# Kernel optimization log

Measured on AMD Instinct MI355X. Metric: run time of the kernel, lower is better.

The kernel has to match this reference:

```python
import jax, jax.numpy as jnp
import numpy as np

B, S, D = 4, 2048, 1024
H = 16
HD = D // H

def setup_inputs() -> dict:
    key = jax.random.key(0)
    ks = jax.random.split(key, 5)
    x = jax.random.normal(ks[0], (B, S, D), dtype=jnp.float32)
    # PyTorch Linear: y = x @ W.T + b; store W in torch layout [out, in]
    w_qkv = jax.random.normal(ks[1], (3 * D, D), dtype=jnp.float32) * (1.0 / np.sqrt(D))
    b_qkv = jax.random.normal(ks[2], (3 * D,), dtype=jnp.float32) * 0.01
    w_out = jax.random.normal(ks[3], (D, D), dtype=jnp.float32) * (1.0 / np.sqrt(D))
    b_out = jax.random.normal(ks[4], (D,), dtype=jnp.float32) * 0.01
    return {"x": x, "w_qkv": w_qkv, "b_qkv": b_qkv, "w_out": w_out, "b_out": b_out}

def reference(x, w_qkv, b_qkv, w_out, b_out):
    b, s, d = x.shape
    qkv = x @ w_qkv.T + b_qkv                      # [B,S,3D]
    q, k, v = jnp.split(qkv, 3, axis=2)
    # [B,S,D] -> [B,H,S,HD]
    q = q.reshape(b, s, H, HD).transpose(0, 2, 1, 3)
    k = k.reshape(b, s, H, HD).transpose(0, 2, 1, 3)
    v = v.reshape(b, s, H, HD).transpose(0, 2, 1, 3)
    att = jnp.einsum('bhqd,bhkd->bhqk', q, k) / np.sqrt(HD)
    causal = jnp.tril(jnp.ones((s, s), dtype=bool))
    att = jnp.where(causal[None, None], att, -jnp.inf)
    att = jax.nn.softmax(att, axis=-1)
    y = jnp.einsum('bhqk,bhkd->bhqd', att, v)      # [B,H,S,HD]
    y = y.transpose(0, 2, 1, 3).reshape(b, s, d)
    return y @ w_out.T + b_out
```

## Files before the change

### kernel.cpp

```cpp
#include <hip/hip_runtime.h>
#include <hip/hip_bf16.h>

#define DEV __device__ __forceinline__

typedef __attribute__((ext_vector_type(8))) short bf16x8;
typedef __attribute__((ext_vector_type(4))) float f32x4;

#define BB 4
#define SS 2048
#define DD 1024
#define HH 16
#define HDD 64
#define MM (BB * SS)
#define NT (SS / 64)
#define NQT (SS / 128)

DEV short f2bf(float f) {
  unsigned u = __builtin_bit_cast(unsigned, f);
  u = u + 0x7fffu + ((u >> 16) & 1u);
  return (short)(u >> 16);
}

DEV float fexp2(float x) {
  float r;
  asm("v_exp_f32 %0, %1" : "=v"(r) : "v"(x));
  return r;
}
DEV float frcp(float x) {
  float r;
  asm("v_rcp_f32 %0, %1" : "=v"(r) : "v"(x));
  return r;
}
DEV unsigned cvtpk(float a, float b) {
  unsigned r;
  asm("v_cvt_pk_bf16_f32 %0, %1, %2" : "=v"(r) : "v"(a), "v"(b));
  return r;
}

DEV void gload_lds16(const void* g, void* l) {
  __builtin_amdgcn_global_load_lds((const __attribute__((address_space(1))) void*)g,
                                   (__attribute__((address_space(3))) void*)l, 16, 0, 0);
}

DEV void cast_range(const float* __restrict__ in, unsigned long long* __restrict__ out,
                    int n4, int start, int stride) {
  for (int i = start; i < n4; i += stride) {
    const float4 f = ((const float4*)in)[i];
    unsigned long long a = (unsigned long long)(unsigned short)f2bf(f.x)
        | ((unsigned long long)(unsigned short)f2bf(f.y) << 16)
        | ((unsigned long long)(unsigned short)f2bf(f.z) << 32)
        | ((unsigned long long)(unsigned short)f2bf(f.w) << 48);
    out[i] = a;
  }
}

__global__ __launch_bounds__(256)
void cast3_f32_bf16(const float* __restrict__ x, unsigned long long* __restrict__ ox, int nx4,
                    const float* __restrict__ wq, unsigned long long* __restrict__ owq, int nwq4,
                    const float* __restrict__ wo, unsigned long long* __restrict__ owo, int nwo4) {
  const int start = blockIdx.x * 256 + threadIdx.x;
  const int stride = gridDim.x * 256;
  cast_range(x, ox, nx4, start, stride);
  cast_range(wq, owq, nwq4, start, stride);
  cast_range(wo, owo, nwo4, start, stride);
}

template<int EPI>
__global__ __launch_bounds__(256)
void gemm_bt(const short* __restrict__ A, const short* __restrict__ Bw,
             const float* __restrict__ bias,
             short* __restrict__ qo, short* __restrict__ ko, short* __restrict__ vo,
             float* __restrict__ co,
             int M, int N, int K) {
  __shared__ short sA[128 * 64];
  __shared__ short sB[128 * 64];
  const int lane = threadIdx.x & 63;
  const int wv = threadIdx.x >> 6;
  const int wm = wv >> 1, wn = wv & 1;
  const int m0 = blockIdx.y * 128;
  const int n0 = blockIdx.x * 128;
  f32x4 acc[4][4] = {};
  const int nkt = K >> 6;
  for (int kt = 0; kt < nkt; ++kt) {
    const int k0 = kt << 6;
    if (kt) __syncthreads();
#pragma unroll
    for (int i = 0; i < 4; ++i) {
      const int c = i * 4 + wv;
      const int b = c * 1024 + lane * 16;
      const int row = b >> 7;
      const int colb = b & 127;
      gload_lds16((const char*)A + ((size_t)(m0 + row) * K + k0) * 2 + colb,
                  (char*)sA + c * 1024);
      gload_lds16((const char*)Bw + ((size_t)(n0 + row) * K + k0) * 2 + colb,
                  (char*)sB + c * 1024);
    }
    __syncthreads();
#pragma unroll
    for (int ks = 0; ks < 2; ++ks) {
      bf16x8 af[4], bf_[4];
#pragma unroll
      for (int i = 0; i < 4; ++i) {
        af[i]  = *(const bf16x8*)&sA[(wm * 64 + i * 16 + (lane & 15)) * 64 + ks * 32 + (lane >> 4) * 8];
        bf_[i] = *(const bf16x8*)&sB[(wn * 64 + i * 16 + (lane & 15)) * 64 + ks * 32 + (lane >> 4) * 8];
      }
#pragma unroll
      for (int i = 0; i < 4; ++i)
#pragma unroll
        for (int j = 0; j < 4; ++j)
          acc[i][j] = __builtin_amdgcn_mfma_f32_16x16x32_bf16(af[i], bf_[j], acc[i][j], 0, 0, 0);
    }
  }
#pragma unroll
  for (int i = 0; i < 4; ++i) {
#pragma unroll
    for (int j = 0; j < 4; ++j) {
#pragma unroll
      for (int r = 0; r < 4; ++r) {
        const int row = m0 + wm * 64 + i * 16 + (lane >> 4) * 4 + r;
        const int col = n0 + wn * 64 + j * 16 + (lane & 15);
        float v = acc[i][j][r] + bias[col];
        if (EPI == 0) {
          const int part = col >> 10, oo = col & 1023;
          const int h = oo >> 6, d = oo & 63;
          const int bb = row >> 11, s = row & 2047;
          if (part == 0)
            qo[(((size_t)bb * HH + h) * SS + s) * HDD + d] = f2bf(v * 0.18033688f);
          else if (part == 1)
            ko[(((size_t)bb * HH + h) * SS + s) * HDD + d] = f2bf(v);
          else {
            const int q = (s >> 2) & 15;
            const int tau = (q & 8) | ((q & 3) << 1) | ((q >> 2) & 1);
            vo[(((size_t)bb * HH + h) * HDD + d) * SS + (s & ~63) + (tau << 2) + (s & 3)] = f2bf(v);
          }
        } else {
          co[(size_t)row * N + col] = v;
        }
      }
    }
  }
}

__global__ __launch_bounds__(256)
void attn_fwd(const short* __restrict__ Q, const short* __restrict__ K,
              const short* __restrict__ V, short* __restrict__ Y) {
  __shared__ short sK[2][64 * 64];
  __shared__ short sV[2][64 * 64];
  const int bh = blockIdx.y;
  const int tid = threadIdx.x, lane = tid & 63, w = tid >> 6;
  const size_t bqk = (size_t)bh * (SS * HDD);
  const size_t bv  = (size_t)bh * (HDD * SS);
  const int b = bh >> 4, h = bh & 15;
  const int lr = lane & 15;
  const int lg = lane >> 4;
  const int lm = lr & 7;

  const int e0 = w * 64 + lane;
  const int e1 = 256 + e0;
  const int r0 = e0 >> 3, s0 = ((e0 & 7) ^ (r0 & 7)) * 8;
  const int r1 = e1 >> 3, s1 = ((e1 & 7) ^ (r1 & 7)) * 8;

  for (int qsel = 0; qsel < 2; ++qsel) {
    const int qt = qsel ? (NQT - 1 - blockIdx.x) : blockIdx.x;
    const int q0 = qt * 128;
    const int nkv = 2 * qt + 2;

    __syncthreads();

    {
      const short* gK = K + bqk;
      const short* gV = V + bv;
      gload_lds16(gK + (size_t)r0 * HDD + s0, &sK[0][e0 * 8]);
      gload_lds16(gV + (size_t)r0 * SS + s0, &sV[0][e0 * 8]);
      gload_lds16(gK + (size_t)r1 * HDD + s1, &sK[0][e1 * 8]);
      gload_lds16(gV + (size_t)r1 * SS + s1, &sV[0][e1 * 8]);
    }

    const int qbase = q0 + w * 32;
    bf16x8 qf[2][2];
#pragma unroll
    for (int g = 0; g < 2; ++g)
#pragma unroll
      for (int ks = 0; ks < 2; ++ks)
        qf[g][ks] = *(const bf16x8*)&Q[bqk + (size_t)(qbase + g * 16 + lr) * HDD + ks * 32 + lg * 8];

    f32x4 accO[2][4] = {};
    float m_[2] = {-1e30f, -1e30f}, l_[2] = {0.f, 0.f};

    int cur = 0;
    for (int kt = 0; kt < nkv; ++kt) {
      const int kc0 = kt * 64;
      __syncthreads();
      if (kt < nkv - 1) {
        const short* gK = K + bqk + (size_t)(kc0 + 64) * 64;
        const short* gV = V + bv + kc0 + 64;
        gload_lds16(gK + (size_t)r0 * HDD + s0, &sK[cur ^ 1][e0 * 8]);
        gload_lds16(gV + (size_t)r0 * SS + s0, &sV[cur ^ 1][e0 * 8]);
        gload_lds16(gK + (size_t)r1 * HDD + s1, &sK[cur ^ 1][e1 * 8]);
        gload_lds16(gV + (size_t)r1 * SS + s1, &sV[cur ^ 1][e1 * 8]);
      }

      f32x4 st[2][4] = {};
#pragma unroll
      for (int ks = 0; ks < 2; ++ks) {
#pragma unroll
        for (int nf = 0; nf < 4; ++nf) {
          const int row = nf * 16 + lr;
          const bf16x8 kf = *(const bf16x8*)&sK[cur][row * 64 + (((ks << 2) + lg) ^ lm) * 8];
          st[0][nf] = __builtin_amdgcn_mfma_f32_16x16x32_bf16(kf, qf[0][ks], st[0][nf], 0, 0, 0);
          st[1][nf] = __builtin_amdgcn_mfma_f32_16x16x32_bf16(kf, qf[1][ks], st[1][nf], 0, 0, 0);
        }
      }
      if (kt >= nkv - 2) {
#pragma unroll
        for (int g = 0; g < 2; ++g) {
          const int q = qbase + g * 16 + lr;
#pragma unroll
          for (int nf = 0; nf < 4; ++nf)
#pragma unroll
            for (int r = 0; r < 4; ++r) {
              const int k = kc0 + nf * 16 + lg * 4 + r;
              if (k > q) st[g][nf][r] = -1e30f;
            }
        }
      }

      unsigned u[2][4][2];
#pragma unroll
      for (int g = 0; g < 2; ++g) {
        float rm = -1e30f;
#pragma unroll
        for (int r = 0; r < 4; ++r)
          rm = fmaxf(rm, fmaxf(fmaxf(st[g][0][r], st[g][1][r]), fmaxf(st[g][2][r], st[g][3][r])));
        rm = fmaxf(rm, __shfl_xor(rm, 16));
        rm = fmaxf(rm, __shfl_xor(rm, 32));

        const bool need = rm > m_[g] + 11.5416f;
        if (__any(need)) {
          const float mn = fmaxf(m_[g], rm);
          const float scale = fexp2(m_[g] - mn);
          m_[g] = mn;
          l_[g] *= scale;
#pragma unroll
          for (int r = 0; r < 4; ++r) {
            const float scl = __shfl(scale, (lane & 48) + (lg << 2) + r);
#pragma unroll
            for (int df = 0; df < 4; ++df) accO[g][df][r] *= scl;
          }
        }

        float rs = 0.f;
#pragma unroll
        for (int nf = 0; nf < 4; ++nf)
#pragma unroll
          for (int r = 0; r < 4; ++r) {
            const float p = fexp2(st[g][nf][r] - m_[g]);
            st[g][nf][r] = p;
            rs += p;
          }
        rs += __shfl_xor(rs, 16);
        rs += __shfl_xor(rs, 32);
        l_[g] += rs;

#pragma unroll
        for (int nf = 0; nf < 4; ++nf) {
          u[g][nf][0] = cvtpk(st[g][nf][0], st[g][nf][1]);
          u[g][nf][1] = cvtpk(st[g][nf][2], st[g][nf][3]);
        }
      }

#pragma unroll
      for (int c = 0; c < 2; ++c) {
        int4 pw0, pw1;
        pw0.x = (int)u[0][2 * c][0]; pw0.y = (int)u[0][2 * c][1];
        pw0.z = (int)u[0][2 * c + 1][0]; pw0.w = (int)u[0][2 * c + 1][1];
        pw1.x = (int)u[1][2 * c][0]; pw1.y = (int)u[1][2 * c][1];
        pw1.z = (int)u[1][2 * c + 1][0]; pw1.w = (int)u[1][2 * c + 1][1];
        const bf16x8 pf0 = __builtin_bit_cast(bf16x8, pw0);
        const bf16x8 pf1 = __builtin_bit_cast(bf16x8, pw1);
        const int slot = (((c << 2) + lg) ^ lm) * 8;
#pragma unroll
        for (int df = 0; df < 4; ++df) {
          const bf16x8 vf = *(const bf16x8*)&sV[cur][(df * 16 + lr) * 64 + slot];
          accO[0][df] = __builtin_amdgcn_mfma_f32_16x16x32_bf16(pf0, vf, accO[0][df], 0, 0, 0);
          accO[1][df] = __builtin_amdgcn_mfma_f32_16x16x32_bf16(pf1, vf, accO[1][df], 0, 0, 0);
        }
      }
      cur ^= 1;
    }

#pragma unroll
    for (int g = 0; g < 2; ++g)
#pragma unroll
      for (int r = 0; r < 4; ++r) {
        const float lv = __shfl(l_[g], (lane & 48) + (lg << 2) + r);
        const float inv = frcp(lv);
        const int srow = qbase + g * 16 + lg * 4 + r;
#pragma unroll
        for (int df = 0; df < 4; ++df) {
          const int dcol = h * HDD + df * 16 + lr;
          Y[((size_t)b * SS + srow) * DD + dcol] = f2bf(accO[g][df][r] * inv);
        }
      }
  }
}

extern "C" void kernel_launch(void* const* d_in, const int* in_sizes, int n_in,
                              void* d_out, int out_size, void* d_ws, size_t ws_size,
                              hipStream_t stream) {
  const float* x     = (const float*)d_in[0];
  const float* w_qkv = (const float*)d_in[1];
  const float* b_qkv = (const float*)d_in[2];
  const float* w_out = (const float*)d_in[3];
  const float* b_out = (const float*)d_in[4];
  float* out = (float*)d_out;

  const size_t nx = (size_t)MM * DD;
  const size_t nwq = (size_t)3 * DD * DD;
  const size_t nwo = (size_t)DD * DD;

  short* x_bf    = (short*)d_ws;
  short* wqkv_bf = x_bf + nx;
  short* wout_bf = wqkv_bf + nwq;
  short* q_ws    = wout_bf + nwo;
  short* k_ws    = q_ws + nx;
  short* v_ws    = k_ws + nx;
  short* y_ws    = v_ws + nx;

  cast3_f32_bf16<<<dim3(2048), dim3(256), 0, stream>>>(
      x, (unsigned long long*)x_bf, (int)(nx / 4),
      w_qkv, (unsigned long long*)wqkv_bf, (int)(nwq / 4),
      w_out, (unsigned long long*)wout_bf, (int)(nwo / 4));

  gemm_bt<0><<<dim3(3 * DD / 128, MM / 128), dim3(256), 0, stream>>>(
      x_bf, wqkv_bf, b_qkv, q_ws, k_ws, v_ws, nullptr, MM, 3 * DD, DD);

  attn_fwd<<<dim3(NQT / 2, BB * HH), dim3(256), 0, stream>>>(q_ws, k_ws, v_ws, y_ws);

  gemm_bt<1><<<dim3(DD / 128, MM / 128), dim3(256), 0, stream>>>(
      y_ws, wout_bf, b_out, nullptr, nullptr, nullptr, out, MM, DD, DD);
}
```

Baseline: 200.6 us.

## Double-buffer GEMM LDS tiles and XOR-swizzle layout to avoid bank conflicts

```diff
diff --git a/kernel.cpp b/kernel.cpp
--- a/kernel.cpp
+++ b/kernel.cpp
@@ -72,37 +72,55 @@
              short* __restrict__ qo, short* __restrict__ ko, short* __restrict__ vo,
              float* __restrict__ co,
              int M, int N, int K) {
-  __shared__ short sA[128 * 64];
-  __shared__ short sB[128 * 64];
+  __shared__ short sA[2][128 * 64];
+  __shared__ short sB[2][128 * 64];
   const int lane = threadIdx.x & 63;
   const int wv = threadIdx.x >> 6;
   const int wm = wv >> 1, wn = wv & 1;
   const int m0 = blockIdx.y * 128;
   const int n0 = blockIdx.x * 128;
+  const int lr = lane & 15;
+  const int lg = lane >> 4;
+  const int lm = lr & 7;
+
+  int srow[4], soff[4], doff[4];
+#pragma unroll
+  for (int i = 0; i < 4; ++i) {
+    const int e = (i * 4 + wv) * 64 + lane;
+    const int row = e >> 3;
+    srow[i] = row;
+    soff[i] = ((e & 7) ^ (row & 7)) * 8;
+    doff[i] = e * 8;
+  }
+
   f32x4 acc[4][4] = {};
   const int nkt = K >> 6;
+
+#pragma unroll
+  for (int i = 0; i < 4; ++i) {
+    gload_lds16(A  + (size_t)(m0 + srow[i]) * K + soff[i], &sA[0][doff[i]]);
+    gload_lds16(Bw + (size_t)(n0 + srow[i]) * K + soff[i], &sB[0][doff[i]]);
+  }
+
+  int cur = 0;
   for (int kt = 0; kt < nkt; ++kt) {
-    const int k0 = kt << 6;
-    if (kt) __syncthreads();
-#pragma unroll
-    for (int i = 0; i < 4; ++i) {
-      const int c = i * 4 + wv;
-      const int b = c * 1024 + lane * 16;
-      const int row = b >> 7;
-      const int colb = b & 127;
-      gload_lds16((const char*)A + ((size_t)(m0 + row) * K + k0) * 2 + colb,
-                  (char*)sA + c * 1024);
-      gload_lds16((const char*)Bw + ((size_t)(n0 + row) * K + k0) * 2 + colb,
-                  (char*)sB + c * 1024);
-    }
     __syncthreads();
+    if (kt + 1 < nkt) {
+      const int k1 = (kt + 1) << 6;
+#pragma unroll
+      for (int i = 0; i < 4; ++i) {
+        gload_lds16(A  + (size_t)(m0 + srow[i]) * K + k1 + soff[i], &sA[cur ^ 1][doff[i]]);
+        gload_lds16(Bw + (size_t)(n0 + srow[i]) * K + k1 + soff[i], &sB[cur ^ 1][doff[i]]);
+      }
+    }
 #pragma unroll
     for (int ks = 0; ks < 2; ++ks) {
+      const int slot = (((ks << 2) + lg) ^ lm) * 8;
       bf16x8 af[4], bf_[4];
 #pragma unroll
       for (int i = 0; i < 4; ++i) {
-        af[i]  = *(const bf16x8*)&sA[(wm * 64 + i * 16 + (lane & 15)) * 64 + ks * 32 + (lane >> 4) * 8];
-        bf_[i] = *(const bf16x8*)&sB[(wn * 64 + i * 16 + (lane & 15)) * 64 + ks * 32 + (lane >> 4) * 8];
+        af[i]  = *(const bf16x8*)&sA[cur][(wm * 64 + i * 16 + lr) * 64 + slot];
+        bf_[i] = *(const bf16x8*)&sB[cur][(wn * 64 + i * 16 + lr) * 64 + slot];
       }
 #pragma unroll
       for (int i = 0; i < 4; ++i)
@@ -110,15 +128,17 @@
         for (int j = 0; j < 4; ++j)
           acc[i][j] = __builtin_amdgcn_mfma_f32_16x16x32_bf16(af[i], bf_[j], acc[i][j], 0, 0, 0);
     }
-  }
+    cur ^= 1;
+  }
+
 #pragma unroll
   for (int i = 0; i < 4; ++i) {
 #pragma unroll
     for (int j = 0; j < 4; ++j) {
 #pragma unroll
       for (int r = 0; r < 4; ++r) {
-        const int row = m0 + wm * 64 + i * 16 + (lane >> 4) * 4 + r;
-        const int col = n0 + wn * 64 + j * 16 + (lane & 15);
+        const int row = m0 + wm * 64 + i * 16 + lg * 4 + r;
+        const int col = n0 + wn * 64 + j * 16 + lr;
         float v = acc[i][j][r] + bias[col];
         if (EPI == 0) {
           const int part = col >> 10, oo = col & 1023;
@@ -295,11 +315,11 @@
       for (int r = 0; r < 4; ++r) {
         const float lv = __shfl(l_[g], (lane & 48) + (lg << 2) + r);
         const float inv = frcp(lv);
-        const int srow = qbase + g * 16 + lg * 4 + r;
+        const int srow2 = qbase + g * 16 + lg * 4 + r;
 #pragma unroll
         for (int df = 0; df < 4; ++df) {
           const int dcol = h * HDD + df * 16 + lr;
-          Y[((size_t)b * SS + srow) * DD + dcol] = f2bf(accO[g][df][r] * inv);
+          Y[((size_t)b * SS + srow2) * DD + dcol] = f2bf(accO[g][df][r] * inv);
         }
       }
   }
```

Result: no change. 198.2 us (-1.2%).
